# Performance work log

Measured on AMD Instinct MI355X. Metric: run time of the kernel, lower is better.

## Reference

```python
import jax, jax.numpy as jnp
import numpy as np

B, N, CIN, COUT = 4, 4096, 64, 64

def setup_inputs() -> dict:
    key = jax.random.key(0)
    k1, k2, k3, k4, k5 = jax.random.split(key, 5)
    X = jax.random.normal(k1, (B, N, CIN), dtype=jnp.float32)
    A = jax.random.uniform(k2, (N, N), dtype=jnp.float32)
    weight1 = jax.random.normal(k3, (CIN, COUT), dtype=jnp.float32) * 0.05
    weight2 = jax.random.normal(k4, (1 * COUT, COUT), dtype=jnp.float32) * 0.05
    alpha = jax.random.normal(k5, (2 * COUT, 1), dtype=jnp.float32) * 0.05
    return {"X": X, "A": A, "weight1": weight1, "weight2": weight2, "alpha": alpha}

def reference(X, A, weight1, weight2, alpha):
    n = A.shape[0]
    c = weight1.shape[1]
    b = X.shape[0]
    # add self loops on the adjacency diagonal
    idx = jnp.arange(n)
    adj = A.at[idx, idx].set(1.0)
    # node transform: [B,N,C]
    out = jnp.matmul(X, weight1)
    # edge feature (P=1): [N,N,1], row-normalized over j (axis=1)
    E = adj[:, :, None]
    E_wave = E / E.sum(axis=1, keepdims=True)
    # attention scores via rank-1 decomposition of alpha
    att_l = jnp.matmul(out, alpha[:c])   # [B,N,1]
    att_r = jnp.matmul(out, alpha[c:])   # [B,N,1]
    scores = jax.nn.leaky_relu(att_l @ jnp.swapaxes(att_r, 1, 2))  # [B,N,N]
    # exp + edge-feature weighting: [P,B,N,N]
    att = jnp.einsum('bij,ijp->pbij', jnp.exp(scores), E_wave)
    # manual softmax-style normalization over neighbors j
    att = att / att.sum(axis=-1, keepdims=True)
    # aggregate: [B,N,P,C] -> [B,N,P*C]
    agg = jnp.einsum('pbij,bjc->bipc', att, out).reshape(b, n, -1)
    return jnp.matmul(agg, weight2)
```

## Files before the change

### kernel.cpp

```cpp
#include <hip/hip_runtime.h>
#include <hip/hip_bf16.h>

typedef __attribute__((ext_vector_type(8))) short short8;
typedef __attribute__((ext_vector_type(4))) float floatx4;
typedef unsigned int u32;

#define NN 4096

static __device__ __forceinline__ unsigned f2bf_rne(float x) {
    union { float f; unsigned u; } v; v.f = x;
    unsigned r = v.u + 0x7fffu + ((v.u >> 16) & 1u);
    return r >> 16;
}
static __device__ __forceinline__ float bf2f(unsigned hi) {
    union { unsigned u; float f; } v; v.u = hi << 16; return v.f;
}

__global__ __launch_bounds__(256, 4)
void prep_kernel(const float* __restrict__ X,
                 const float* __restrict__ W1,
                 const float* __restrict__ W2,
                 const float* __restrict__ alpha,
                 unsigned short* __restrict__ Gt,
                 float* __restrict__ lv,
                 float* __restrict__ rv) {
    __shared__ __align__(16) char sm[53248];
    float* W1s  = (float*)sm;
    float* W2s  = (float*)(sm + 17408);
    float* Wcst = (float*)(sm + 34816);
    float* w1s  = (float*)(sm + 52224);
    float* als  = (float*)(sm + 52736);
    float* GsT  = (float*)sm;

    const int t = threadIdx.x;
    const int row0 = blockIdx.x * 64;
    const int b = row0 >> 12, n0 = row0 & (NN - 1);
    const int w = t >> 6, lane = t & 63;
    const int m = lane & 15, q = lane >> 4;

    const int row = row0 + w * 16 + m;
    const float* xp = X + (size_t)row * 64;
    float4 x0 = *(const float4*)(xp + q * 8);
    float4 x1 = *(const float4*)(xp + q * 8 + 4);
    float4 x2 = *(const float4*)(xp + 32 + q * 8);
    float4 x3 = *(const float4*)(xp + 32 + q * 8 + 4);

    #pragma unroll
    for (int s = 0; s < 4; ++s) {
        int idx = s * 1024 + t * 4;
        int r = idx >> 6, cc = idx & 63;
        *(float4*)&W1s[r * 68 + cc] = *(const float4*)(W1 + idx);
        *(float4*)&W2s[r * 68 + cc] = *(const float4*)(W2 + idx);
    }
    if (t < 128) als[t] = alpha[t];
    __syncthreads();

    {
        const int k = t >> 2, nq = t & 3;
        float acc[16];
        #pragma unroll
        for (int i = 0; i < 16; ++i) acc[i] = 0.f;
        for (int mm = 0; mm < 64; ++mm) {
            float w1v = W1s[k * 68 + mm];
            #pragma unroll
            for (int i = 0; i < 16; ++i)
                acc[i] += w1v * W2s[mm * 68 + nq * 16 + i];
        }
        #pragma unroll
        for (int i = 0; i < 16; ++i)
            Wcst[(nq * 16 + i) * 68 + k] = acc[i];
    }
    if (t < 64) {
        float sl = 0.f, sr = 0.f;
        for (int cc2 = 0; cc2 < 64; ++cc2) {
            float wv = W1s[t * 68 + cc2];
            sl += wv * als[cc2];
            sr += wv * als[64 + cc2];
        }
        w1s[t] = sl; w1s[64 + t] = sr;
    }
    __syncthreads();

    const float xs[16] = {x0.x,x0.y,x0.z,x0.w, x1.x,x1.y,x1.z,x1.w,
                          x2.x,x2.y,x2.z,x2.w, x3.x,x3.y,x3.z,x3.w};

    float pl = 0.f, pr = 0.f;
    #pragma unroll
    for (int ks = 0; ks < 2; ++ks)
        #pragma unroll
        for (int j = 0; j < 8; ++j) {
            int k = ks * 32 + q * 8 + j;
            float xv = xs[ks * 8 + j];
            pl += xv * w1s[k];
            pr += xv * w1s[64 + k];
        }
    pl += __shfl_xor(pl, 16, 64); pl += __shfl_xor(pl, 32, 64);
    pr += __shfl_xor(pr, 16, 64); pr += __shfl_xor(pr, 32, 64);
    if (q == 0) { lv[row] = pl; rv[row] = pr; }

    short8 ah[2], al[2];
    #pragma unroll
    for (int ks = 0; ks < 2; ++ks)
        #pragma unroll
        for (int j = 0; j < 8; ++j) {
            float f = xs[ks * 8 + j];
            unsigned hb = f2bf_rne(f);
            float res = f - bf2f(hb);
            ah[ks][j] = (short)hb;
            al[ks][j] = (short)f2bf_rne(res);
        }

    short8 bfr[4][2];
    #pragma unroll
    for (int nt = 0; nt < 4; ++nt)
        #pragma unroll
        for (int ks = 0; ks < 2; ++ks) {
            const float* wp = &Wcst[(nt * 16 + m) * 68 + ks * 32 + q * 8];
            float4 w0 = *(const float4*)wp;
            float4 w1 = *(const float4*)(wp + 4);
            short8 bf;
            bf[0] = (short)f2bf_rne(w0.x); bf[1] = (short)f2bf_rne(w0.y);
            bf[2] = (short)f2bf_rne(w0.z); bf[3] = (short)f2bf_rne(w0.w);
            bf[4] = (short)f2bf_rne(w1.x); bf[5] = (short)f2bf_rne(w1.y);
            bf[6] = (short)f2bf_rne(w1.z); bf[7] = (short)f2bf_rne(w1.w);
            bfr[nt][ks] = bf;
        }

    floatx4 acc[4] = {{0,0,0,0},{0,0,0,0},{0,0,0,0},{0,0,0,0}};
    #pragma unroll
    for (int ks = 0; ks < 2; ++ks)
        #pragma unroll
        for (int nt = 0; nt < 4; ++nt) {
            acc[nt] = __builtin_amdgcn_mfma_f32_16x16x32_bf16(ah[ks], bfr[nt][ks], acc[nt], 0, 0, 0);
            acc[nt] = __builtin_amdgcn_mfma_f32_16x16x32_bf16(al[ks], bfr[nt][ks], acc[nt], 0, 0, 0);
        }

    __syncthreads();
    #pragma unroll
    for (int nt = 0; nt < 4; ++nt)
        #pragma unroll
        for (int rg = 0; rg < 4; ++rg)
            GsT[(nt * 16 + m) * 68 + w * 16 + q * 4 + rg] = acc[nt][rg];
    __syncthreads();
    unsigned* Gu = (unsigned*)Gt;
    #pragma unroll
    for (int it2 = 0; it2 < 8; ++it2) {
        int c2 = (t >> 5) + it2 * 8;
        int np = t & 31;
        unsigned lo = f2bf_rne(GsT[c2 * 68 + 2 * np]);
        unsigned hi = f2bf_rne(GsT[c2 * 68 + 2 * np + 1]);
        Gu[(((((size_t)(b * 64 + c2)) << 12) + n0) >> 1) + np] = lo | (hi << 16);
    }
}

__global__ __launch_bounds__(256, 4)
void attn_main(const float* __restrict__ A,
               const unsigned short* __restrict__ Gt,
               const float* __restrict__ lv,
               const float* __restrict__ rv,
               float* __restrict__ pout) {
    __shared__ __align__(16) float rs[1024];
    __shared__ __align__(16) unsigned short Gs[2][64 * 40];

    const int bx = blockIdx.x;
    const int grp = bx & 3;
    const int it  = (bx >> 2) & 63;
    const int b   = bx >> 8;
    const int i0  = it * 64;
    const int t = threadIdx.x;
    const int wsub = t >> 6, lane = t & 63;
    const int m = lane & 15, q = lane >> 4;
    const int irow = wsub * 16 + m;

    *(float4*)&rs[t * 4] = *(const float4*)(rv + (size_t)b * NN + grp * 1024 + t * 4);

    const float* aRow = A + (size_t)(i0 + irow) * NN + grp * 1024 + q * 8;
    const int sc = t >> 2, jj = (t & 3) * 8;
    const unsigned short* gStage = Gt + (((size_t)(b * 64 + sc)) << 12) + grp * 1024 + jj;

    const float li = lv[b * NN + i0 + irow] * 1.44269504f;
    const float li001 = li * 0.01f;

    short8 s0 = *(const short8*)(gStage);
    short8 sA = *(const short8*)(gStage + 32);
    short8 sB = *(const short8*)(gStage + 64);
    float4 a0A = *(const float4*)(aRow);
    float4 a1A = *(const float4*)(aRow + 4);
    float4 a0B = *(const float4*)(aRow + 32);
    float4 a1B = *(const float4*)(aRow + 36);

    const bool diag_grp = ((i0 >> 10) == grp);
    const int jd = (i0 + irow) - grp * 1024;

    floatx4 acc0 = {0,0,0,0}, acc1 = {0,0,0,0}, acc2 = {0,0,0,0}, acc3 = {0,0,0,0};
    float dsum = 0.f;

    *(short8*)&Gs[0][sc * 40 + jj] = s0;
    __syncthreads();

    auto genE = [&](float4 a0, float4 a1, int chunk) -> short8 {
        float aa[8] = {a0.x, a0.y, a0.z, a0.w, a1.x, a1.y, a1.z, a1.w};
        if (diag_grp && ((jd >> 5) == chunk)) {
            const int dd = jd - (chunk * 32 + q * 8);
            #pragma unroll
            for (int e = 0; e < 8; ++e) if (dd == e) aa[e] = 1.0f;
        }
        const float4 r0 = *(const float4*)&rs[chunk * 32 + q * 8];
        const float4 r1 = *(const float4*)&rs[chunk * 32 + q * 8 + 4];
        const float rr[8] = {r0.x, r0.y, r0.z, r0.w, r1.x, r1.y, r1.z, r1.w};
        unsigned up[8];
        #pragma unroll
        for (int e = 0; e < 8; ++e) {
            float s = fmaxf(li * rr[e], li001 * rr[e]);
            float ev = __builtin_amdgcn_exp2f(s) * aa[e];
            unsigned u = __float_as_uint(ev) + 0x8000u;
            up[e] = u;
            dsum += __uint_as_float(u & 0xffff0000u);
        }
        union { unsigned u[4]; short8 s8; } cv;
        cv.u[0] = __builtin_amdgcn_perm(up[1], up[0], 0x07060302u);
        cv.u[1] = __builtin_amdgcn_perm(up[3], up[2], 0x07060302u);
        cv.u[2] = __builtin_amdgcn_perm(up[5], up[4], 0x07060302u);
        cv.u[3] = __builtin_amdgcn_perm(up[7], up[6], 0x07060302u);
        return cv.s8;
    };

    for (int cc = 0; cc < 32; cc += 2) {
        {
            *(short8*)&Gs[1][sc * 40 + jj] = sA;
            { const int jn = (cc + 3 < 32) ? (cc + 3) * 32 : 0;
              sA = *(const short8*)(gStage + jn); }
            const short8 afr = genE(a0A, a1A, cc);
            { const int jn = (cc + 2 < 32) ? (cc + 2) * 32 : 0;
              a0A = *(const float4*)(aRow + jn);
              a1A = *(const float4*)(aRow + jn + 4); }
            const short8 b0 = *(const short8*)&Gs[0][( m) * 40 + q * 8];
            const short8 b1 = *(const short8*)&Gs[0][(16 + m) * 40 + q * 8];
            const short8 b2 = *(const short8*)&Gs[0][(32 + m) * 40 + q * 8];
            const short8 b3 = *(const short8*)&Gs[0][(48 + m) * 40 + q * 8];
            acc0 = __builtin_amdgcn_mfma_f32_16x16x32_bf16(afr, b0, acc0, 0, 0, 0);
            acc1 = __builtin_amdgcn_mfma_f32_16x16x32_bf16(afr, b1, acc1, 0, 0, 0);
            acc2 = __builtin_amdgcn_mfma_f32_16x16x32_bf16(afr, b2, acc2, 0, 0, 0);
            acc3 = __builtin_amdgcn_mfma_f32_16x16x32_bf16(afr, b3, acc3, 0, 0, 0);
            __syncthreads();
        }
        {
            *(short8*)&Gs[0][sc * 40 + jj] = sB;
            { const int jn = (cc + 4 < 32) ? (cc + 4) * 32 : 0;
              sB = *(const short8*)(gStage + jn); }
            const short8 afr = genE(a0B, a1B, cc + 1);
            { const int jn = (cc + 3 < 32) ? (cc + 3) * 32 : 0;
              a0B = *(const float4*)(aRow + jn);
              a1B = *(const float4*)(aRow + jn + 4); }
            const short8 b0 = *(const short8*)&Gs[1][( m) * 40 + q * 8];
            const short8 b1 = *(const short8*)&Gs[1][(16 + m) * 40 + q * 8];
            const short8 b2 = *(const short8*)&Gs[1][(32 + m) * 40 + q * 8];
            const short8 b3 = *(const short8*)&Gs[1][(48 + m) * 40 + q * 8];
            acc0 = __builtin_amdgcn_mfma_f32_16x16x32_bf16(afr, b0, acc0, 0, 0, 0);
            acc1 = __builtin_amdgcn_mfma_f32_16x16x32_bf16(afr, b1, acc1, 0, 0, 0);
            acc2 = __builtin_amdgcn_mfma_f32_16x16x32_bf16(afr, b2, acc2, 0, 0, 0);
            acc3 = __builtin_amdgcn_mfma_f32_16x16x32_bf16(afr, b3, acc3, 0, 0, 0);
            __syncthreads();
        }
    }

    dsum += __shfl_xor(dsum, 16, 64);
    dsum += __shfl_xor(dsum, 32, 64);

    float* pb = pout + (size_t)bx * (64 * 68);
    #pragma unroll
    for (int nt = 0; nt < 4; ++nt) {
        floatx4 av = nt == 0 ? acc0 : nt == 1 ? acc1 : nt == 2 ? acc2 : acc3;
        #pragma unroll
        for (int rg = 0; rg < 4; ++rg)
            pb[(wsub * 16 + q * 4 + rg) * 68 + nt * 16 + m] = av[rg];
    }
    if (q == 0) pb[(wsub * 16 + m) * 68 + 64] = dsum;
}

__global__ __launch_bounds__(256, 4)
void attn_reduce(const float* __restrict__ pout,
                 float* __restrict__ out) {
    const int bx = blockIdx.x;
    const int it = bx & 63, b = bx >> 6;
    const int t = threadIdx.x;
    const int row = t >> 2, quad = t & 3;

    const float* base = pout + (size_t)((b * 64 + it) * 4) * (64 * 68);
    float den = 0.f;
    #pragma unroll
    for (int p = 0; p < 4; ++p)
        den += base[p * 4352 + row * 68 + 64];
    const float rinv = 1.0f / den;

    float* op = out + (((size_t)(b * NN + it * 64 + row)) << 6) + quad * 16;
    #pragma unroll
    for (int f = 0; f < 4; ++f) {
        float4 s = {0.f, 0.f, 0.f, 0.f};
        #pragma unroll
        for (int p = 0; p < 4; ++p) {
            const float4 v = *(const float4*)&base[p * 4352 + row * 68 + quad * 16 + f * 4];
            s.x += v.x; s.y += v.y; s.z += v.z; s.w += v.w;
        }
        float4 o;
        o.x = s.x * rinv; o.y = s.y * rinv; o.z = s.z * rinv; o.w = s.w * rinv;
        *(float4*)(op + f * 4) = o;
    }
}

extern "C" void kernel_launch(void* const* d_in, const int* in_sizes, int n_in,
                              void* d_out, int out_size, void* d_ws, size_t ws_size,
                              hipStream_t stream) {
    const float* X     = (const float*)d_in[0];
    const float* A     = (const float*)d_in[1];
    const float* W1    = (const float*)d_in[2];
    const float* W2    = (const float*)d_in[3];
    const float* alpha = (const float*)d_in[4];
    float* out = (float*)d_out;

    char* ws = (char*)d_ws;
    unsigned short* Gt = (unsigned short*)(ws);
    float* lvp  = (float*)(ws + 2097152);
    float* rvp  = (float*)(ws + 2097152 + 65536);
    float* pout = (float*)(ws + 2097152 + 131072);

    prep_kernel<<<256, 256, 0, stream>>>(X, W1, W2, alpha, Gt, lvp, rvp);
    attn_main<<<1024, 256, 0, stream>>>(A, Gt, lvp, rvp, pout);
    attn_reduce<<<256, 256, 0, stream>>>(pout, out);
}
```

Before: 160.5 us.

## Use single-wave 16-row blocks with batch-adjacent scheduling to reuse A in cache

```diff
diff --git a/kernel.cpp b/kernel.cpp
--- a/kernel.cpp
+++ b/kernel.cpp
@@ -153,60 +153,73 @@
     }
 }
 
-__global__ __launch_bounds__(256, 4)
+__global__ __launch_bounds__(64, 4)
 void attn_main(const float* __restrict__ A,
                const unsigned short* __restrict__ Gt,
                const float* __restrict__ lv,
                const float* __restrict__ rv,
                float* __restrict__ pout) {
-    __shared__ __align__(16) float rs[1024];
-    __shared__ __align__(16) unsigned short Gs[2][64 * 40];
+    __shared__ __align__(16) unsigned short Gs[2][64 * 36];
 
     const int bx = blockIdx.x;
-    const int grp = bx & 3;
-    const int it  = (bx >> 2) & 63;
-    const int b   = bx >> 8;
-    const int i0  = it * 64;
+    const int b    = bx & 3;
+    const int grp  = (bx >> 2) & 3;
+    const int it16 = bx >> 4;
+    const int i0   = it16 * 16;
     const int t = threadIdx.x;
-    const int wsub = t >> 6, lane = t & 63;
-    const int m = lane & 15, q = lane >> 4;
-    const int irow = wsub * 16 + m;
-
-    *(float4*)&rs[t * 4] = *(const float4*)(rv + (size_t)b * NN + grp * 1024 + t * 4);
-
-    const float* aRow = A + (size_t)(i0 + irow) * NN + grp * 1024 + q * 8;
-    const int sc = t >> 2, jj = (t & 3) * 8;
-    const unsigned short* gStage = Gt + (((size_t)(b * 64 + sc)) << 12) + grp * 1024 + jj;
-
-    const float li = lv[b * NN + i0 + irow] * 1.44269504f;
+    const int m = t & 15, q = t >> 4;
+
+    const float* aRow = A + (size_t)(i0 + m) * NN + grp * 1024 + q * 8;
+    const float* rvp  = rv + (size_t)b * NN + grp * 1024 + q * 8;
+    const unsigned short* gSt = Gt + (((size_t)(b * 64 + t)) << 12) + grp * 1024;
+
+    const float li = lv[b * NN + i0 + m] * 1.44269504f;
     const float li001 = li * 0.01f;
 
-    short8 s0 = *(const short8*)(gStage);
-    short8 sA = *(const short8*)(gStage + 32);
-    short8 sB = *(const short8*)(gStage + 64);
-    float4 a0A = *(const float4*)(aRow);
-    float4 a1A = *(const float4*)(aRow + 4);
-    float4 a0B = *(const float4*)(aRow + 32);
-    float4 a1B = *(const float4*)(aRow + 36);
-
     const bool diag_grp = ((i0 >> 10) == grp);
-    const int jd = (i0 + irow) - grp * 1024;
+    const int jd = (i0 + m) - grp * 1024;
+
+    short8 sg0 = *(const short8*)(gSt);
+    short8 sg1 = *(const short8*)(gSt + 8);
+    short8 sg2 = *(const short8*)(gSt + 16);
+    short8 sg3 = *(const short8*)(gSt + 24);
+    *(short8*)&Gs[0][t * 36 + 0]  = sg0;
+    *(short8*)&Gs[0][t * 36 + 8]  = sg1;
+    *(short8*)&Gs[0][t * 36 + 16] = sg2;
+    *(short8*)&Gs[0][t * 36 + 24] = sg3;
+    sg0 = *(const short8*)(gSt + 32);
+    sg1 = *(const short8*)(gSt + 40);
+    sg2 = *(const short8*)(gSt + 48);
+    sg3 = *(const short8*)(gSt + 56);
+    float4 a0 = *(const float4*)(aRow);
+    float4 a1 = *(const float4*)(aRow + 4);
+    float4 r0 = *(const float4*)(rvp);
+    float4 r1 = *(const float4*)(rvp + 4);
 
     floatx4 acc0 = {0,0,0,0}, acc1 = {0,0,0,0}, acc2 = {0,0,0,0}, acc3 = {0,0,0,0};
     float dsum = 0.f;
 
-    *(short8*)&Gs[0][sc * 40 + jj] = s0;
-    __syncthreads();
-
-    auto genE = [&](float4 a0, float4 a1, int chunk) -> short8 {
+    #pragma unroll 2
+    for (int cc = 0; cc < 32; ++cc) {
+        {
+            unsigned short* wp = &Gs[(cc + 1) & 1][t * 36];
+            *(short8*)(wp + 0)  = sg0;
+            *(short8*)(wp + 8)  = sg1;
+            *(short8*)(wp + 16) = sg2;
+            *(short8*)(wp + 24) = sg3;
+        }
+        { const int jn = (cc + 2 < 32) ? (cc + 2) * 32 : 0;
+          sg0 = *(const short8*)(gSt + jn);
+          sg1 = *(const short8*)(gSt + jn + 8);
+          sg2 = *(const short8*)(gSt + jn + 16);
+          sg3 = *(const short8*)(gSt + jn + 24); }
+
         float aa[8] = {a0.x, a0.y, a0.z, a0.w, a1.x, a1.y, a1.z, a1.w};
-        if (diag_grp && ((jd >> 5) == chunk)) {
-            const int dd = jd - (chunk * 32 + q * 8);
+        if (diag_grp && ((jd >> 5) == cc)) {
+            const int dd = jd - (cc * 32 + q * 8);
             #pragma unroll
             for (int e = 0; e < 8; ++e) if (dd == e) aa[e] = 1.0f;
         }
-        const float4 r0 = *(const float4*)&rs[chunk * 32 + q * 8];
-        const float4 r1 = *(const float4*)&rs[chunk * 32 + q * 8 + 4];
         const float rr[8] = {r0.x, r0.y, r0.z, r0.w, r1.x, r1.y, r1.z, r1.w};
         unsigned up[8];
         #pragma unroll
@@ -222,88 +235,72 @@
         cv.u[1] = __builtin_amdgcn_perm(up[3], up[2], 0x07060302u);
         cv.u[2] = __builtin_amdgcn_perm(up[5], up[4], 0x07060302u);
         cv.u[3] = __builtin_amdgcn_perm(up[7], up[6], 0x07060302u);
-        return cv.s8;
-    };
-
-    for (int cc = 0; cc < 32; cc += 2) {
+        const short8 afr = cv.s8;
+
+        { const int jn = (cc + 1 < 32) ? (cc + 1) * 32 : 0;
+          a0 = *(const float4*)(aRow + jn);
+          a1 = *(const float4*)(aRow + jn + 4);
+          r0 = *(const float4*)(rvp + jn);
+          r1 = *(const float4*)(rvp + jn + 4); }
+
         {
-            *(short8*)&Gs[1][sc * 40 + jj] = sA;
-            { const int jn = (cc + 3 < 32) ? (cc + 3) * 32 : 0;
-              sA = *(const short8*)(gStage + jn); }
-            const short8 afr = genE(a0A, a1A, cc);
-            { const int jn = (cc + 2 < 32) ? (cc + 2) * 32 : 0;
-              a0A = *(const float4*)(aRow + jn);
-              a1A = *(const float4*)(aRow + jn + 4); }
-            const short8 b0 = *(const short8*)&Gs[0][( m) * 40 + q * 8];
-            const short8 b1 = *(const short8*)&Gs[0][(16 + m) * 40 + q * 8];
-            const short8 b2 = *(const short8*)&Gs[0][(32 + m) * 40 + q * 8];
-            const short8 b3 = *(const short8*)&Gs[0][(48 + m) * 40 + q * 8];
+            const unsigned short* rp = &Gs[cc & 1][0];
+            const short8 b0 = *(const short8*)&rp[( m) * 36 + q * 8];
+            const short8 b1 = *(const short8*)&rp[(16 + m) * 36 + q * 8];
+            const short8 b2 = *(const short8*)&rp[(32 + m) * 36 + q * 8];
+            const short8 b3 = *(const short8*)&rp[(48 + m) * 36 + q * 8];
             acc0 = __builtin_amdgcn_mfma_f32_16x16x32_bf16(afr, b0, acc0, 0, 0, 0);
             acc1 = __builtin_amdgcn_mfma_f32_16x16x32_bf16(afr, b1, acc1, 0, 0, 0);
             acc2 = __builtin_amdgcn_mfma_f32_16x16x32_bf16(afr, b2, acc2, 0, 0, 0);
             acc3 = __builtin_amdgcn_mfma_f32_16x16x32_bf16(afr, b3, acc3, 0, 0, 0);
-            __syncthreads();
-        }
-        {
-            *(short8*)&Gs[0][sc * 40 + jj] = sB;
-            { const int jn = (cc + 4 < 32) ? (cc + 4) * 32 : 0;
-              sB = *(const short8*)(gStage + jn); }
-            const short8 afr = genE(a0B, a1B, cc + 1);
-            { const int jn = (cc + 3 < 32) ? (cc + 3) * 32 : 0;
-              a0B = *(const float4*)(aRow + jn);
-              a1B = *(const float4*)(aRow + jn + 4); }
-            const short8 b0 = *(const short8*)&Gs[1][( m) * 40 + q * 8];
-            const short8 b1 = *(const short8*)&Gs[1][(16 + m) * 40 + q * 8];
-            const short8 b2 = *(const short8*)&Gs[1][(32 + m) * 40 + q * 8];
-            const short8 b3 = *(const short8*)&Gs[1][(48 + m) * 40 + q * 8];
-            acc0 = __builtin_amdgcn_mfma_f32_16x16x32_bf16(afr, b0, acc0, 0, 0, 0);
-            acc1 = __builtin_amdgcn_mfma_f32_16x16x32_bf16(afr, b1, acc1, 0, 0, 0);
-            acc2 = __builtin_amdgcn_mfma_f32_16x16x32_bf16(afr, b2, acc2, 0, 0, 0);
-            acc3 = __builtin_amdgcn_mfma_f32_16x16x32_bf16(afr, b3, acc3, 0, 0, 0);
-            __syncthreads();
         }
     }
 
     dsum += __shfl_xor(dsum, 16, 64);
     dsum += __shfl_xor(dsum, 32, 64);
 
-    float* pb = pout + (size_t)bx * (64 * 68);
+    float* pb = pout + (size_t)bx * (16 * 68);
     #pragma unroll
     for (int nt = 0; nt < 4; ++nt) {
         floatx4 av = nt == 0 ? acc0 : nt == 1 ? acc1 : nt == 2 ? acc2 : acc3;
         #pragma unroll
         for (int rg = 0; rg < 4; ++rg)
-            pb[(wsub * 16 + q * 4 + rg) * 68 + nt * 16 + m] = av[rg];
-    }
-    if (q == 0) pb[(wsub * 16 + m) * 68 + 64] = dsum;
+            pb[(q * 4 + rg) * 68 + nt * 16 + m] = av[rg];
+    }
+    if (q == 0) pb[m * 68 + 64] = dsum;
 }
 
 __global__ __launch_bounds__(256, 4)
 void attn_reduce(const float* __restrict__ pout,
                  float* __restrict__ out) {
     const int bx = blockIdx.x;
-    const int it = bx & 63, b = bx >> 6;
+    const int it64 = bx & 63, b = bx >> 6;
     const int t = threadIdx.x;
-    const int row = t >> 2, quad = t & 3;
-
-    const float* base = pout + (size_t)((b * 64 + it) * 4) * (64 * 68);
-    float den = 0.f;
-    #pragma unroll
-    for (int p = 0; p < 4; ++p)
-        den += base[p * 4352 + row * 68 + 64];
+    const int r64 = t >> 2, quad = t & 3;
+
+    const int it16 = (it64 << 2) + (r64 >> 4);
+    const int rr = r64 & 15;
+
+    const float* base0 = pout + ((size_t)(((it16 * 4) + 0) * 4 + b)) * 1088 + rr * 68;
+    const float* base1 = pout + ((size_t)(((it16 * 4) + 1) * 4 + b)) * 1088 + rr * 68;
+    const float* base2 = pout + ((size_t)(((it16 * 4) + 2) * 4 + b)) * 1088 + rr * 68;
+    const float* base3 = pout + ((size_t)(((it16 * 4) + 3) * 4 + b)) * 1088 + rr * 68;
+
+    float den = base0[64] + base1[64] + base2[64] + base3[64];
     const float rinv = 1.0f / den;
 
-    float* op = out + (((size_t)(b * NN + it * 64 + row)) << 6) + quad * 16;
+    float* op = out + (((size_t)(b * NN + it64 * 64 + r64)) << 6) + quad * 16;
     #pragma unroll
     for (int f = 0; f < 4; ++f) {
-        float4 s = {0.f, 0.f, 0.f, 0.f};
-        #pragma unroll
-        for (int p = 0; p < 4; ++p) {
-            const float4 v = *(const float4*)&base[p * 4352 + row * 68 + quad * 16 + f * 4];
-            s.x += v.x; s.y += v.y; s.z += v.z; s.w += v.w;
-        }
+        const float4 v0 = *(const float4*)&base0[quad * 16 + f * 4];
+        const float4 v1 = *(const float4*)&base1[quad * 16 + f * 4];
+        const float4 v2 = *(const float4*)&base2[quad * 16 + f * 4];
+        const float4 v3 = *(const float4*)&base3[quad * 16 + f * 4];
         float4 o;
-        o.x = s.x * rinv; o.y = s.y * rinv; o.z = s.z * rinv; o.w = s.w * rinv;
+        o.x = (v0.x + v1.x + v2.x + v3.x) * rinv;
+        o.y = (v0.y + v1.y + v2.y + v3.y) * rinv;
+        o.z = (v0.z + v1.z + v2.z + v3.z) * rinv;
+        o.w = (v0.w + v1.w + v2.w + v3.w) * rinv;
         *(float4*)(op + f * 4) = o;
     }
 }
@@ -325,6 +322,6 @@
     float* pout = (float*)(ws + 2097152 + 131072);
 
     prep_kernel<<<256, 256, 0, stream>>>(X, W1, W2, alpha, Gt, lvp, rvp);
-    attn_main<<<1024, 256, 0, stream>>>(A, Gt, lvp, rvp, pout);
+    attn_main<<<4096, 64, 0, stream>>>(A, Gt, lvp, rvp, pout);
     attn_reduce<<<256, 256, 0, stream>>>(pout, out);
 }
```

Result: slower. 218.9 us (+36.4%).
